# Kernel tuning notes

Hardware: AMD Instinct MI355X
Metric: run time of the kernel (lower is better)

## Reference

```python
import jax, jax.numpy as jnp
import numpy as np

DIM = 1024
E = 8
TOP_K = 2
HID = int(DIM * 2.68)  # 2744


def setup_inputs() -> dict:
    key = jax.random.key(0)
    ks = jax.random.split(key, 8)
    s = 0.02
    return {
        "x": jax.random.normal(ks[0], (4, 1024, DIM), dtype=jnp.float32),
        "gate_w": jax.random.normal(ks[1], (E, DIM), dtype=jnp.float32) * s,
        "w1": jax.random.normal(ks[2], (E, HID, DIM), dtype=jnp.float32) * s,
        "w2": jax.random.normal(ks[3], (E, HID, DIM), dtype=jnp.float32) * s,
        "w3": jax.random.normal(ks[4], (E, DIM, HID), dtype=jnp.float32) * s,
        "sw1": jax.random.normal(ks[5], (HID, DIM), dtype=jnp.float32) * s,
        "sw2": jax.random.normal(ks[6], (HID, DIM), dtype=jnp.float32) * s,
        "sw3": jax.random.normal(ks[7], (DIM, HID), dtype=jnp.float32) * s,
    }


def reference(x, gate_w, w1, w2, w3, sw1, sw2, sw3):
    B, T, C = x.shape
    xf = x.reshape(-1, C)  # [S, C]
    logits = xf @ gate_w.T  # [S, E]
    rw = jax.nn.softmax(logits.astype(jnp.float32), axis=-1)
    tkw, tki = jax.lax.top_k(rw, TOP_K)  # [S, K]
    nE = rw.shape[-1]
    importance = rw.mean(0)  # [E]
    load = jax.nn.one_hot(tki[:, 0], nE, dtype=jnp.float32).mean(0)  # [E]
    aux_loss = nE * (importance * load).sum()
    tkw = tkw / tkw.sum(-1, keepdims=True)
    tkw = tkw.astype(x.dtype)
    # dense all-expert SwiGLU (faithful to original: every expert on every token)
    h = jax.nn.silu(jnp.einsum('sc,ehc->seh', xf, w1)) * jnp.einsum('sc,ehc->seh', xf, w2)  # [S,E,H]
    eo = jnp.einsum('seh,ech->sec', h, w3)  # [S, E, C]
    sel = jnp.take_along_axis(eo, tki[:, :, None], axis=1)  # [S, K, C]
    weighted = (sel * tkw[:, :, None]).sum(1)  # [S, C]
    shared = (jax.nn.silu(xf @ sw1.T) * (xf @ sw2.T)) @ sw3.T  # [S, C]
    y = (weighted + shared).reshape(B, T, C)
    return y, aux_loss
```

## Files before the change

### kernel.cpp

```cpp
#include <hip/hip_runtime.h>
#include <cstdio>
#include <cstdint>

#define S_TOK 4096
#define CDIM  1024
#define EXP   8
#define HRAW  2744
#define HPAD  2816
#define MAXROWS  13312
#define MAXTILES 104
#define NSLICE1  (HPAD / 128)
#define NSLICE2  (CDIM / 256)

typedef __attribute__((ext_vector_type(8))) short bf16x8;
typedef __attribute__((ext_vector_type(4))) float f32x4;
typedef __attribute__((ext_vector_type(4))) unsigned short us4;
typedef unsigned short us;

__device__ __forceinline__ us f2bf(float f) {
  unsigned u = __float_as_uint(f);
  u += 0x7fffu + ((u >> 16) & 1u);
  return (us)(u >> 16);
}

__device__ __forceinline__ void gl16(const us* g, us* l) {
  __builtin_amdgcn_global_load_lds((__attribute__((address_space(1))) void*)g,
                                   (__attribute__((address_space(3))) void*)l,
                                   16, 0, 0);
}

__device__ __forceinline__ int xcd_swz(int orig, int nwg) {
  int q = nwg >> 3, r = nwg & 7;
  int x = orig & 7, idx = orig >> 3;
  return (x < r ? x * (q + 1) : r * (q + 1) + (x - r) * q) + idx;
}

#define CH_RP1  (HPAD * CDIM / 4)
#define CH_CPR  (HPAD / 4)
#define R_W1    (8 * CH_RP1)
#define R_W2    (R_W1 + 8 * CH_RP1)
#define R_W3    (R_W2 + 8 * CDIM * CH_CPR)
#define R_SW1   (R_W3 + CH_RP1)
#define R_SW2   (R_SW1 + CH_RP1)
#define R_SW3   (R_SW2 + CDIM * CH_CPR)
#define GATE_BLKS (S_TOK / 4)
#define CVT_BLKS  2048

__device__ __forceinline__ void cvt4_rowpad(const float* __restrict__ src,
                                            us* __restrict__ dst, int idx) {
  int m = idx / CH_RP1, rem = idx - m * CH_RP1;
  int r = rem >> 8, c4 = rem & 255;
  us4 o;
  if (r < HRAW) {
    float4 v = *(const float4*)(src + ((size_t)(m * HRAW + r) * CDIM + c4 * 4));
    o.x = f2bf(v.x); o.y = f2bf(v.y); o.z = f2bf(v.z); o.w = f2bf(v.w);
  } else { o.x = 0; o.y = 0; o.z = 0; o.w = 0; }
  *(us4*)(dst + ((size_t)(m * HPAD + r) * CDIM + c4 * 4)) = o;
}

__device__ __forceinline__ void cvt4_colpad(const float* __restrict__ src,
                                            us* __restrict__ dst, int idx) {
  int r = idx / CH_CPR, c4 = idx - r * CH_CPR;
  int c = c4 * 4;
  us4 o;
  if (c < HRAW) {
    float4 v = *(const float4*)(src + (size_t)r * HRAW + c);
    o.x = f2bf(v.x); o.y = f2bf(v.y); o.z = f2bf(v.z); o.w = f2bf(v.w);
  } else { o.x = 0; o.y = 0; o.z = 0; o.w = 0; }
  *(us4*)(dst + (size_t)r * HPAD + c) = o;
}

__global__ void __launch_bounds__(256) cvtgate_kernel(
    const float* __restrict__ x, const float* __restrict__ gw,
    const float* __restrict__ w1, const float* __restrict__ w2,
    const float* __restrict__ w3, const float* __restrict__ sw1,
    const float* __restrict__ sw2, const float* __restrict__ sw3,
    us* __restrict__ xb, us* __restrict__ w1b, us* __restrict__ w2b,
    us* __restrict__ w3b, us* __restrict__ sw1b, us* __restrict__ sw2b,
    us* __restrict__ sw3b, int* __restrict__ tki, float* __restrict__ tkw,
    float* __restrict__ probs) {
  if (blockIdx.x < GATE_BLKS) {
    const int wv = threadIdx.x >> 6, lane = threadIdx.x & 63;
    const int s = blockIdx.x * 4 + wv;
    const float4* xs4 = (const float4*)(x + (size_t)s * CDIM);
    float acc[8] = {0, 0, 0, 0, 0, 0, 0, 0};
#pragma unroll
    for (int j = 0; j < 4; j++) {
      float4 v = xs4[lane * 4 + j];
      int c = lane * 16 + j * 4;
      us4 ov;
      ov.x = f2bf(v.x); ov.y = f2bf(v.y); ov.z = f2bf(v.z); ov.w = f2bf(v.w);
      *(us4*)(xb + (size_t)s * CDIM + c) = ov;
#pragma unroll
      for (int ee = 0; ee < 8; ee++) {
        const float* g = gw + ee * CDIM + c;
        acc[ee] += v.x * g[0] + v.y * g[1] + v.z * g[2] + v.w * g[3];
      }
    }
#pragma unroll
    for (int ee = 0; ee < 8; ee++) {
#pragma unroll
      for (int off = 32; off > 0; off >>= 1) acc[ee] += __shfl_xor(acc[ee], off, 64);
    }
    if (lane == 0) {
      float mx = acc[0];
      for (int ee = 1; ee < 8; ee++) mx = fmaxf(mx, acc[ee]);
      float p[8], sm = 0.f;
      for (int ee = 0; ee < 8; ee++) { p[ee] = expf(acc[ee] - mx); sm += p[ee]; }
      float inv = 1.f / sm;
      for (int ee = 0; ee < 8; ee++) probs[s * 8 + ee] = p[ee] * inv;
      int i0 = 0; float b0 = p[0];
      for (int ee = 1; ee < 8; ee++) if (p[ee] > b0) { b0 = p[ee]; i0 = ee; }
      int i1 = -1; float b1 = -1.f;
      for (int ee = 0; ee < 8; ee++) if (ee != i0 && p[ee] > b1) { b1 = p[ee]; i1 = ee; }
      float rw0 = b0 * inv, rw1 = b1 * inv;
      float den = 1.f / (rw0 + rw1);
      tki[2 * s] = i0; tki[2 * s + 1] = i1;
      tkw[2 * s] = rw0 * den; tkw[2 * s + 1] = rw1 * den;
    }
  } else {
    for (int i = (blockIdx.x - GATE_BLKS) * 256 + threadIdx.x; i < R_SW3;
         i += CVT_BLKS * 256) {
      if (i < R_W1)       cvt4_rowpad(w1,  w1b,  i);
      else if (i < R_W2)  cvt4_rowpad(w2,  w2b,  i - R_W1);
      else if (i < R_W3)  cvt4_colpad(w3,  w3b,  i - R_W2);
      else if (i < R_SW1) cvt4_rowpad(sw1, sw1b, i - R_W3);
      else if (i < R_SW2) cvt4_rowpad(sw2, sw2b, i - R_SW1);
      else                cvt4_colpad(sw3, sw3b, i - R_SW2);
    }
  }
}

__global__ void __launch_bounds__(512) build_kernel(const int* __restrict__ tki,
                                                    const float* __restrict__ tkw,
                                                    const float* __restrict__ probs,
                                                    int* __restrict__ meta,
                                                    int* __restrict__ pairtok,
                                                    float* __restrict__ pairw,
                                                    int* __restrict__ invmap,
                                                    int* __restrict__ tile_expert,
                                                    float* __restrict__ aux_out) {
  const int tid = threadIdx.x, lane = tid & 63, wv = tid >> 6;
  __shared__ int s_cnt[EXP];
  __shared__ int s_amc[EXP];
  __shared__ float s_imp[EXP];
  {
    const int e = wv;
    int c_cnt = 0, c_amc = 0;
    float imp = 0.f;
    for (int s0 = 0; s0 < S_TOK; s0 += 64) {
      int s = s0 + lane;
      int i0 = tki[2 * s], i1 = tki[2 * s + 1];
      c_cnt += (i0 == e) || (i1 == e);
      c_amc += (i0 == e);
      imp += probs[s * 8 + e];
    }
#pragma unroll
    for (int off = 32; off > 0; off >>= 1) {
      c_cnt += __shfl_xor(c_cnt, off, 64);
      c_amc += __shfl_xor(c_amc, off, 64);
      imp   += __shfl_xor(imp, off, 64);
    }
    if (lane == 0) { s_cnt[e] = c_cnt; s_amc[e] = c_amc; s_imp[e] = imp; }
  }
  __syncthreads();
  int pad[EXP], start[EXP];
  int o = S_TOK;
#pragma unroll
  for (int j = 0; j < EXP; j++) {
    pad[j] = ((s_cnt[j] + 127) >> 7) << 7;
    start[j] = o;
    o += pad[j];
  }
  const int total = o;
  for (int r = tid; r < S_TOK; r += 512) { pairtok[r] = r; pairw[r] = 1.f; }
  {
    const int e = wv;
    int base = start[e];
    for (int s0 = 0; s0 < S_TOK; s0 += 64) {
      int s = s0 + lane;
      int i0 = tki[2 * s], i1 = tki[2 * s + 1];
      bool m0 = (i0 == e), m1 = (i1 == e);
      bool mm = m0 || m1;
      unsigned long long mk = __ballot(mm);
      if (mm) {
        int pos = base + __popcll(mk & ((1ull << lane) - 1ull));
        pairtok[pos] = s;
        pairw[pos] = m0 ? tkw[2 * s] : tkw[2 * s + 1];
        invmap[2 * s + (m0 ? 0 : 1)] = pos;
      }
      base += __popcll(mk);
    }
    for (int r = base + lane; r < start[e] + pad[e]; r += 64) {
      pairtok[r] = -1; pairw[r] = 0.f;
    }
  }
  if (tid < 128) {
    int ex = 8;
    if (tid >= 32) {
      int rr = tid * 128;
#pragma unroll
      for (int j = 0; j < EXP; j++)
        if (rr >= start[j] && rr < start[j] + pad[j]) ex = j;
    }
    tile_expert[tid] = ex;
  }
  if (tid == 0) {
    meta[0] = total >> 7;
    float a = 0.f;
    for (int j = 0; j < EXP; j++)
      a += (s_imp[j] * (1.f / 4096.f)) * ((float)s_amc[j] * (1.f / 4096.f));
    aux_out[0] = 8.f * a;
  }
}

__global__ void __launch_bounds__(256, 2) gemm1_kernel(
    const us* __restrict__ xb, const us* __restrict__ w1b, const us* __restrict__ w2b,
    const us* __restrict__ sw1b, const us* __restrict__ sw2b,
    const int* __restrict__ pairtok, const int* __restrict__ tile_expert,
    const int* __restrict__ meta, us* __restrict__ h) {
  const int wgid = xcd_swz(blockIdx.x, MAXTILES * NSLICE1);
  const int mt = wgid % MAXTILES;
  if (mt >= meta[0]) return;
  const int n0 = (wgid / MAXTILES) * 128;
  const int e = tile_expert[mt];
  const us* B1 = (e == 8) ? sw1b : (w1b + (size_t)e * HPAD * CDIM);
  const us* B2 = (e == 8) ? sw2b : (w2b + (size_t)e * HPAD * CDIM);
  const int row0 = mt * 128;
  __shared__ __align__(16) us sA[128 * 32];
  __shared__ __align__(16) us sB1[128 * 32];
  __shared__ __align__(16) us sB2[128 * 32];
  const int tid = threadIdx.x, lane = tid & 63;
  const int wm = tid >> 7, wn = (tid >> 6) & 1;
  const int sub = tid & 3, ra = tid >> 2;
  const int subx = sub ^ ((ra >> 1) & 3);
  int t0 = pairtok[row0 + ra];      if (t0 < 0) t0 = 0;
  int t1 = pairtok[row0 + 64 + ra]; if (t1 < 0) t1 = 0;
  const us* gA0 = xb + (size_t)t0 * CDIM + subx * 8;
  const us* gA1 = xb + (size_t)t1 * CDIM + subx * 8;
  const us* gB1a = B1 + (size_t)(n0 + ra) * CDIM + subx * 8;
  const us* gB1b = B1 + (size_t)(n0 + 64 + ra) * CDIM + subx * 8;
  const us* gB2a = B2 + (size_t)(n0 + ra) * CDIM + subx * 8;
  const us* gB2b = B2 + (size_t)(n0 + 64 + ra) * CDIM + subx * 8;
  f32x4 au[4][4], av[4][4];
#pragma unroll
  for (int m = 0; m < 4; m++)
#pragma unroll
    for (int n = 0; n < 4; n++)
#pragma unroll
      for (int r = 0; r < 4; r++) { au[m][n][r] = 0.f; av[m][n][r] = 0.f; }

  const int rl = lane & 15;
  const int kx = (((lane >> 4) ^ ((lane >> 1) & 3)) << 3);
  for (int k0 = 0; k0 < CDIM; k0 += 32) {
    gl16(gA0 + k0,  &sA[tid * 8]);
    gl16(gA1 + k0,  &sA[(tid + 256) * 8]);
    gl16(gB1a + k0, &sB1[tid * 8]);
    gl16(gB1b + k0, &sB1[(tid + 256) * 8]);
    gl16(gB2a + k0, &sB2[tid * 8]);
    gl16(gB2b + k0, &sB2[(tid + 256) * 8]);
    __syncthreads();
    bf16x8 a[4], b1[4], b2[4];
#pragma unroll
    for (int m = 0; m < 4; m++)
      a[m] = *(const bf16x8*)&sA[(wm * 64 + m * 16 + rl) * 32 + kx];
#pragma unroll
    for (int n = 0; n < 4; n++) {
      b1[n] = *(const bf16x8*)&sB1[(wn * 64 + n * 16 + rl) * 32 + kx];
      b2[n] = *(const bf16x8*)&sB2[(wn * 64 + n * 16 + rl) * 32 + kx];
    }
#pragma unroll
    for (int m = 0; m < 4; m++)
#pragma unroll
      for (int n = 0; n < 4; n++) {
        au[m][n] = __builtin_amdgcn_mfma_f32_16x16x32_bf16(a[m], b1[n], au[m][n], 0, 0, 0);
        av[m][n] = __builtin_amdgcn_mfma_f32_16x16x32_bf16(a[m], b2[n], av[m][n], 0, 0, 0);
      }
    __syncthreads();
  }
  const int rb = (lane >> 4) * 4, cb = lane & 15;
#pragma unroll
  for (int m = 0; m < 4; m++)
#pragma unroll
    for (int n = 0; n < 4; n++)
#pragma unroll
      for (int r = 0; r < 4; r++) {
        int row = row0 + wm * 64 + m * 16 + rb + r;
        int col = n0 + wn * 64 + n * 16 + cb;
        float u = au[m][n][r], v = av[m][n][r];
        float sg = 1.f / (1.f + __expf(-u));
        h[(size_t)row * HPAD + col] = f2bf(u * sg * v);
      }
}

__global__ void __launch_bounds__(256, 2) gemm2_kernel(
    const us* __restrict__ h, const us* __restrict__ w3b, const us* __restrict__ sw3b,
    const int* __restrict__ tile_expert, const int* __restrict__ meta,
    float* __restrict__ eo) {
  const int wgid = xcd_swz(blockIdx.x, MAXTILES * NSLICE2);
  const int mt = wgid % MAXTILES;
  if (mt >= meta[0]) return;
  const int n0 = (wgid / MAXTILES) * 256;
  const int e = tile_expert[mt];
  const us* B = (e == 8) ? sw3b : (w3b + (size_t)e * CDIM * HPAD);
  const int row0 = mt * 128;
  __shared__ __align__(16) us sA[128 * 32];
  __shared__ __align__(16) us sB[256 * 32];
  const int tid = threadIdx.x, lane = tid & 63;
  const int wm = tid >> 7, wn = (tid >> 6) & 1;
  const int sub = tid & 3, ra = tid >> 2;
  const int subx = sub ^ ((ra >> 1) & 3);
  const us* gA0 = h + (size_t)(row0 + ra) * HPAD + subx * 8;
  const us* gA1 = h + (size_t)(row0 + 64 + ra) * HPAD + subx * 8;
  const us* gB0 = B + (size_t)(n0 + ra) * HPAD + subx * 8;
  const us* gB1 = B + (size_t)(n0 + 64 + ra) * HPAD + subx * 8;
  const us* gB2 = B + (size_t)(n0 + 128 + ra) * HPAD + subx * 8;
  const us* gB3 = B + (size_t)(n0 + 192 + ra) * HPAD + subx * 8;
  f32x4 ac[4][8];
#pragma unroll
  for (int m = 0; m < 4; m++)
#pragma unroll
    for (int n = 0; n < 8; n++)
#pragma unroll
      for (int r = 0; r < 4; r++) ac[m][n][r] = 0.f;

  const int rl = lane & 15;
  const int kx = (((lane >> 4) ^ ((lane >> 1) & 3)) << 3);
  for (int k0 = 0; k0 < HPAD; k0 += 32) {
    gl16(gA0 + k0, &sA[tid * 8]);
    gl16(gA1 + k0, &sA[(tid + 256) * 8]);
    gl16(gB0 + k0, &sB[tid * 8]);
    gl16(gB1 + k0, &sB[(tid + 256) * 8]);
    gl16(gB2 + k0, &sB[(tid + 512) * 8]);
    gl16(gB3 + k0, &sB[(tid + 768) * 8]);
    __syncthreads();
    bf16x8 a[4], b[8];
#pragma unroll
    for (int m = 0; m < 4; m++)
      a[m] = *(const bf16x8*)&sA[(wm * 64 + m * 16 + rl) * 32 + kx];
#pragma unroll
    for (int n = 0; n < 8; n++)
      b[n] = *(const bf16x8*)&sB[(wn * 128 + n * 16 + rl) * 32 + kx];
#pragma unroll
    for (int m = 0; m < 4; m++)
#pragma unroll
      for (int n = 0; n < 8; n++)
        ac[m][n] = __builtin_amdgcn_mfma_f32_16x16x32_bf16(a[m], b[n], ac[m][n], 0, 0, 0);
    __syncthreads();
  }
  const int rb = (lane >> 4) * 4, cb = lane & 15;
#pragma unroll
  for (int m = 0; m < 4; m++)
#pragma unroll
    for (int n = 0; n < 8; n++)
#pragma unroll
      for (int r = 0; r < 4; r++) {
        int row = row0 + wm * 64 + m * 16 + rb + r;
        int col = n0 + wn * 128 + n * 16 + cb;
        eo[(size_t)row * CDIM + col] = ac[m][n][r];
      }
}

__global__ void __launch_bounds__(256) combine_kernel(const float* __restrict__ eo,
                                                      const int* __restrict__ invmap,
                                                      const float* __restrict__ pairw,
                                                      float* __restrict__ out) {
  const int s = blockIdx.x;
  const int c = threadIdx.x * 4;
  const int j0 = invmap[2 * s], j1 = invmap[2 * s + 1];
  const float w0 = pairw[j0], w1 = pairw[j1];
  float4 a = *(const float4*)(eo + (size_t)s * CDIM + c);
  float4 b = *(const float4*)(eo + (size_t)j0 * CDIM + c);
  float4 d = *(const float4*)(eo + (size_t)j1 * CDIM + c);
  float4 o;
  o.x = a.x + w0 * b.x + w1 * d.x;
  o.y = a.y + w0 * b.y + w1 * d.y;
  o.z = a.z + w0 * b.z + w1 * d.z;
  o.w = a.w + w0 * b.w + w1 * d.w;
  *(float4*)(out + (size_t)s * CDIM + c) = o;
}

extern "C" void kernel_launch(void* const* d_in, const int* in_sizes, int n_in,
                              void* d_out, int out_size, void* d_ws, size_t ws_size,
                              hipStream_t stream) {
  const float* x   = (const float*)d_in[0];
  const float* gw  = (const float*)d_in[1];
  const float* w1  = (const float*)d_in[2];
  const float* w2  = (const float*)d_in[3];
  const float* w3  = (const float*)d_in[4];
  const float* sw1 = (const float*)d_in[5];
  const float* sw2 = (const float*)d_in[6];
  const float* sw3 = (const float*)d_in[7];
  float* out = (float*)d_out;
  char* ws = (char*)d_ws;
  size_t off = 0;
  auto take = [&](size_t bytes) -> char* {
    char* p = ws + off;
    off = (off + bytes + 255) & ~(size_t)255;
    return p;
  };
  us* xb    = (us*)take((size_t)S_TOK * CDIM * 2);
  us* w1b   = (us*)take((size_t)EXP * HPAD * CDIM * 2);
  us* w2b   = (us*)take((size_t)EXP * HPAD * CDIM * 2);
  us* w3b   = (us*)take((size_t)EXP * CDIM * HPAD * 2);
  us* sw1b  = (us*)take((size_t)HPAD * CDIM * 2);
  us* sw2b  = (us*)take((size_t)HPAD * CDIM * 2);
  us* sw3b  = (us*)take((size_t)CDIM * HPAD * 2);
  us* hbuf  = (us*)take((size_t)MAXROWS * HPAD * 2);
  int* pairtok = (int*)take(MAXROWS * 4);
  float* pairw = (float*)take(MAXROWS * 4);
  int* invmap  = (int*)take(S_TOK * 2 * 4);
  int* tile_expert = (int*)take(128 * 4);
  int* tki = (int*)take(S_TOK * 2 * 4);
  float* tkw = (float*)take(S_TOK * 2 * 4);
  float* probs = (float*)take(S_TOK * EXP * 4);
  int* meta = (int*)take(256);
  float* eo = (float*)w1b;
  if (off > ws_size) {
    fprintf(stderr, "MoE kernel: ws too small, need %zu got %zu\n", off, ws_size);
    return;
  }
  cvtgate_kernel<<<GATE_BLKS + CVT_BLKS, 256, 0, stream>>>(
      x, gw, w1, w2, w3, sw1, sw2, sw3,
      xb, w1b, w2b, w3b, sw1b, sw2b, sw3b, tki, tkw, probs);
  build_kernel<<<1, 512, 0, stream>>>(tki, tkw, probs, meta, pairtok, pairw, invmap,
                                      tile_expert, out + (size_t)S_TOK * CDIM);
  gemm1_kernel<<<MAXTILES * NSLICE1, 256, 0, stream>>>(
      xb, w1b, w2b, sw1b, sw2b, pairtok, tile_expert, meta, hbuf);
  gemm2_kernel<<<MAXTILES * NSLICE2, 256, 0, stream>>>(
      hbuf, w3b, sw3b, tile_expert, meta, eo);
  combine_kernel<<<S_TOK, 256, 0, stream>>>(eo, invmap, pairw, out);
}
```

Measured before the change: 472.0 us.

## Overlap weight conversion with routing build and gemm1 via fused launches

```diff
diff --git a/kernel.cpp b/kernel.cpp
--- a/kernel.cpp
+++ b/kernel.cpp
@@ -11,6 +11,7 @@
 #define MAXTILES 104
 #define NSLICE1  (HPAD / 128)
 #define NSLICE2  (CDIM / 256)
+#define G1_BLKS  (MAXTILES * NSLICE1)
 
 typedef __attribute__((ext_vector_type(8))) short bf16x8;
 typedef __attribute__((ext_vector_type(4))) float f32x4;
@@ -37,14 +38,6 @@
 
 #define CH_RP1  (HPAD * CDIM / 4)
 #define CH_CPR  (HPAD / 4)
-#define R_W1    (8 * CH_RP1)
-#define R_W2    (R_W1 + 8 * CH_RP1)
-#define R_W3    (R_W2 + 8 * CDIM * CH_CPR)
-#define R_SW1   (R_W3 + CH_RP1)
-#define R_SW2   (R_SW1 + CH_RP1)
-#define R_SW3   (R_SW2 + CDIM * CH_CPR)
-#define GATE_BLKS (S_TOK / 4)
-#define CVT_BLKS  2048
 
 __device__ __forceinline__ void cvt4_rowpad(const float* __restrict__ src,
                                             us* __restrict__ dst, int idx) {
@@ -70,156 +63,172 @@
   *(us4*)(dst + (size_t)r * HPAD + c) = o;
 }
 
-__global__ void __launch_bounds__(256) cvtgate_kernel(
-    const float* __restrict__ x, const float* __restrict__ gw,
+__global__ void __launch_bounds__(256) gate_kernel(const float* __restrict__ x,
+                                                   const float* __restrict__ gw,
+                                                   us* __restrict__ xb,
+                                                   int* __restrict__ tki,
+                                                   float* __restrict__ tkw,
+                                                   float* __restrict__ probs) {
+  const int wv = threadIdx.x >> 6, lane = threadIdx.x & 63;
+  const int s = blockIdx.x * 4 + wv;
+  const float4* xs4 = (const float4*)(x + (size_t)s * CDIM);
+  float acc[8] = {0, 0, 0, 0, 0, 0, 0, 0};
+#pragma unroll
+  for (int j = 0; j < 4; j++) {
+    float4 v = xs4[lane * 4 + j];
+    int c = lane * 16 + j * 4;
+    us4 ov;
+    ov.x = f2bf(v.x); ov.y = f2bf(v.y); ov.z = f2bf(v.z); ov.w = f2bf(v.w);
+    *(us4*)(xb + (size_t)s * CDIM + c) = ov;
+#pragma unroll
+    for (int ee = 0; ee < 8; ee++) {
+      const float* g = gw + ee * CDIM + c;
+      acc[ee] += v.x * g[0] + v.y * g[1] + v.z * g[2] + v.w * g[3];
+    }
+  }
+#pragma unroll
+  for (int ee = 0; ee < 8; ee++) {
+#pragma unroll
+    for (int off = 32; off > 0; off >>= 1) acc[ee] += __shfl_xor(acc[ee], off, 64);
+  }
+  if (lane == 0) {
+    float mx = acc[0];
+    for (int ee = 1; ee < 8; ee++) mx = fmaxf(mx, acc[ee]);
+    float p[8], sm = 0.f;
+    for (int ee = 0; ee < 8; ee++) { p[ee] = expf(acc[ee] - mx); sm += p[ee]; }
+    float inv = 1.f / sm;
+    for (int ee = 0; ee < 8; ee++) probs[s * 8 + ee] = p[ee] * inv;
+    int i0 = 0; float b0 = p[0];
+    for (int ee = 1; ee < 8; ee++) if (p[ee] > b0) { b0 = p[ee]; i0 = ee; }
+    int i1 = -1; float b1 = -1.f;
+    for (int ee = 0; ee < 8; ee++) if (ee != i0 && p[ee] > b1) { b1 = p[ee]; i1 = ee; }
+    float rw0 = b0 * inv, rw1 = b1 * inv;
+    float den = 1.f / (rw0 + rw1);
+    tki[2 * s] = i0; tki[2 * s + 1] = i1;
+    tkw[2 * s] = rw0 * den; tkw[2 * s + 1] = rw1 * den;
+  }
+}
+
+#define CVTAB_BLKS 2048
+#define AB_W1   (8 * CH_RP1)
+#define AB_W2   (AB_W1 + 8 * CH_RP1)
+#define AB_SW1  (AB_W2 + CH_RP1)
+#define AB_SW2  (AB_SW1 + CH_RP1)
+
+__global__ void __launch_bounds__(512) cvtab_build_kernel(
     const float* __restrict__ w1, const float* __restrict__ w2,
-    const float* __restrict__ w3, const float* __restrict__ sw1,
-    const float* __restrict__ sw2, const float* __restrict__ sw3,
-    us* __restrict__ xb, us* __restrict__ w1b, us* __restrict__ w2b,
-    us* __restrict__ w3b, us* __restrict__ sw1b, us* __restrict__ sw2b,
-    us* __restrict__ sw3b, int* __restrict__ tki, float* __restrict__ tkw,
-    float* __restrict__ probs) {
-  if (blockIdx.x < GATE_BLKS) {
-    const int wv = threadIdx.x >> 6, lane = threadIdx.x & 63;
-    const int s = blockIdx.x * 4 + wv;
-    const float4* xs4 = (const float4*)(x + (size_t)s * CDIM);
-    float acc[8] = {0, 0, 0, 0, 0, 0, 0, 0};
-#pragma unroll
-    for (int j = 0; j < 4; j++) {
-      float4 v = xs4[lane * 4 + j];
-      int c = lane * 16 + j * 4;
-      us4 ov;
-      ov.x = f2bf(v.x); ov.y = f2bf(v.y); ov.z = f2bf(v.z); ov.w = f2bf(v.w);
-      *(us4*)(xb + (size_t)s * CDIM + c) = ov;
-#pragma unroll
-      for (int ee = 0; ee < 8; ee++) {
-        const float* g = gw + ee * CDIM + c;
-        acc[ee] += v.x * g[0] + v.y * g[1] + v.z * g[2] + v.w * g[3];
-      }
-    }
-#pragma unroll
-    for (int ee = 0; ee < 8; ee++) {
-#pragma unroll
-      for (int off = 32; off > 0; off >>= 1) acc[ee] += __shfl_xor(acc[ee], off, 64);
-    }
-    if (lane == 0) {
-      float mx = acc[0];
-      for (int ee = 1; ee < 8; ee++) mx = fmaxf(mx, acc[ee]);
-      float p[8], sm = 0.f;
-      for (int ee = 0; ee < 8; ee++) { p[ee] = expf(acc[ee] - mx); sm += p[ee]; }
-      float inv = 1.f / sm;
-      for (int ee = 0; ee < 8; ee++) probs[s * 8 + ee] = p[ee] * inv;
-      int i0 = 0; float b0 = p[0];
-      for (int ee = 1; ee < 8; ee++) if (p[ee] > b0) { b0 = p[ee]; i0 = ee; }
-      int i1 = -1; float b1 = -1.f;
-      for (int ee = 0; ee < 8; ee++) if (ee != i0 && p[ee] > b1) { b1 = p[ee]; i1 = ee; }
-      float rw0 = b0 * inv, rw1 = b1 * inv;
-      float den = 1.f / (rw0 + rw1);
-      tki[2 * s] = i0; tki[2 * s + 1] = i1;
-      tkw[2 * s] = rw0 * den; tkw[2 * s + 1] = rw1 * den;
-    }
-  } else {
-    for (int i = (blockIdx.x - GATE_BLKS) * 256 + threadIdx.x; i < R_SW3;
-         i += CVT_BLKS * 256) {
-      if (i < R_W1)       cvt4_rowpad(w1,  w1b,  i);
-      else if (i < R_W2)  cvt4_rowpad(w2,  w2b,  i - R_W1);
-      else if (i < R_W3)  cvt4_colpad(w3,  w3b,  i - R_W2);
-      else if (i < R_SW1) cvt4_rowpad(sw1, sw1b, i - R_W3);
-      else if (i < R_SW2) cvt4_rowpad(sw2, sw2b, i - R_SW1);
-      else                cvt4_colpad(sw3, sw3b, i - R_SW2);
-    }
-  }
-}
-
-__global__ void __launch_bounds__(512) build_kernel(const int* __restrict__ tki,
-                                                    const float* __restrict__ tkw,
-                                                    const float* __restrict__ probs,
-                                                    int* __restrict__ meta,
-                                                    int* __restrict__ pairtok,
-                                                    float* __restrict__ pairw,
-                                                    int* __restrict__ invmap,
-                                                    int* __restrict__ tile_expert,
-                                                    float* __restrict__ aux_out) {
-  const int tid = threadIdx.x, lane = tid & 63, wv = tid >> 6;
-  __shared__ int s_cnt[EXP];
-  __shared__ int s_amc[EXP];
-  __shared__ float s_imp[EXP];
-  {
-    const int e = wv;
-    int c_cnt = 0, c_amc = 0;
-    float imp = 0.f;
-    for (int s0 = 0; s0 < S_TOK; s0 += 64) {
-      int s = s0 + lane;
-      int i0 = tki[2 * s], i1 = tki[2 * s + 1];
-      c_cnt += (i0 == e) || (i1 == e);
-      c_amc += (i0 == e);
-      imp += probs[s * 8 + e];
-    }
-#pragma unroll
-    for (int off = 32; off > 0; off >>= 1) {
-      c_cnt += __shfl_xor(c_cnt, off, 64);
-      c_amc += __shfl_xor(c_amc, off, 64);
-      imp   += __shfl_xor(imp, off, 64);
-    }
-    if (lane == 0) { s_cnt[e] = c_cnt; s_amc[e] = c_amc; s_imp[e] = imp; }
-  }
-  __syncthreads();
-  int pad[EXP], start[EXP];
-  int o = S_TOK;
-#pragma unroll
-  for (int j = 0; j < EXP; j++) {
-    pad[j] = ((s_cnt[j] + 127) >> 7) << 7;
-    start[j] = o;
-    o += pad[j];
-  }
-  const int total = o;
-  for (int r = tid; r < S_TOK; r += 512) { pairtok[r] = r; pairw[r] = 1.f; }
-  {
-    const int e = wv;
-    int base = start[e];
-    for (int s0 = 0; s0 < S_TOK; s0 += 64) {
-      int s = s0 + lane;
-      int i0 = tki[2 * s], i1 = tki[2 * s + 1];
-      bool m0 = (i0 == e), m1 = (i1 == e);
-      bool mm = m0 || m1;
-      unsigned long long mk = __ballot(mm);
-      if (mm) {
-        int pos = base + __popcll(mk & ((1ull << lane) - 1ull));
-        pairtok[pos] = s;
-        pairw[pos] = m0 ? tkw[2 * s] : tkw[2 * s + 1];
-        invmap[2 * s + (m0 ? 0 : 1)] = pos;
-      }
-      base += __popcll(mk);
-    }
-    for (int r = base + lane; r < start[e] + pad[e]; r += 64) {
-      pairtok[r] = -1; pairw[r] = 0.f;
-    }
-  }
-  if (tid < 128) {
-    int ex = 8;
-    if (tid >= 32) {
-      int rr = tid * 128;
-#pragma unroll
+    const float* __restrict__ sw1, const float* __restrict__ sw2,
+    us* __restrict__ w1b, us* __restrict__ w2b,
+    us* __restrict__ sw1b, us* __restrict__ sw2b,
+    const int* __restrict__ tki, const float* __restrict__ tkw,
+    const float* __restrict__ probs, int* __restrict__ meta,
+    int* __restrict__ pairtok, float* __restrict__ pairw,
+    int* __restrict__ invmap, int* __restrict__ tile_expert,
+    float* __restrict__ aux_out) {
+  if (blockIdx.x == 0) {
+    const int tid = threadIdx.x, lane = tid & 63, wv = tid >> 6;
+    __shared__ int s_cnt[EXP];
+    __shared__ int s_amc[EXP];
+    __shared__ float s_imp[EXP];
+    {
+      const int e = wv;
+      int c_cnt = 0, c_amc = 0;
+      float imp = 0.f;
+      for (int s0 = 0; s0 < S_TOK; s0 += 64) {
+        int s = s0 + lane;
+        int i0 = tki[2 * s], i1 = tki[2 * s + 1];
+        c_cnt += (i0 == e) || (i1 == e);
+        c_amc += (i0 == e);
+        imp += probs[s * 8 + e];
+      }
+#pragma unroll
+      for (int off = 32; off > 0; off >>= 1) {
+        c_cnt += __shfl_xor(c_cnt, off, 64);
+        c_amc += __shfl_xor(c_amc, off, 64);
+        imp   += __shfl_xor(imp, off, 64);
+      }
+      if (lane == 0) { s_cnt[e] = c_cnt; s_amc[e] = c_amc; s_imp[e] = imp; }
+    }
+    __syncthreads();
+    int pad[EXP], start[EXP];
+    int o = S_TOK;
+#pragma unroll
+    for (int j = 0; j < EXP; j++) {
+      pad[j] = ((s_cnt[j] + 127) >> 7) << 7;
+      start[j] = o;
+      o += pad[j];
+    }
+    const int total = o;
+    for (int r = tid; r < S_TOK; r += 512) { pairtok[r] = r; pairw[r] = 1.f; }
+    {
+      const int e = wv;
+      int base = start[e];
+      for (int s0 = 0; s0 < S_TOK; s0 += 64) {
+        int s = s0 + lane;
+        int i0 = tki[2 * s], i1 = tki[2 * s + 1];
+        bool m0 = (i0 == e), m1 = (i1 == e);
+        bool mm = m0 || m1;
+        unsigned long long mk = __ballot(mm);
+        if (mm) {
+          int pos = base + __popcll(mk & ((1ull << lane) - 1ull));
+          pairtok[pos] = s;
+          pairw[pos] = m0 ? tkw[2 * s] : tkw[2 * s + 1];
+          invmap[2 * s + (m0 ? 0 : 1)] = pos;
+        }
+        base += __popcll(mk);
+      }
+      for (int r = base + lane; r < start[e] + pad[e]; r += 64) {
+        pairtok[r] = -1; pairw[r] = 0.f;
+      }
+    }
+    if (tid < 128) {
+      int ex = 8;
+      if (tid >= 32) {
+        int rr = tid * 128;
+#pragma unroll
+        for (int j = 0; j < EXP; j++)
+          if (rr >= start[j] && rr < start[j] + pad[j]) ex = j;
+      }
+      tile_expert[tid] = ex;
+    }
+    if (tid == 0) {
+      meta[0] = total >> 7;
+      float a = 0.f;
       for (int j = 0; j < EXP; j++)
-        if (rr >= start[j] && rr < start[j] + pad[j]) ex = j;
-    }
-    tile_expert[tid] = ex;
-  }
-  if (tid == 0) {
-    meta[0] = total >> 7;
-    float a = 0.f;
-    for (int j = 0; j < EXP; j++)
-      a += (s_imp[j] * (1.f / 4096.f)) * ((float)s_amc[j] * (1.f / 4096.f));
-    aux_out[0] = 8.f * a;
-  }
-}
+        a += (s_imp[j] * (1.f / 4096.f)) * ((float)s_amc[j] * (1.f / 4096.f));
+      aux_out[0] = 8.f * a;
+    }
+    return;
+  }
+  for (int i = (blockIdx.x - 1) * 512 + threadIdx.x; i < AB_SW2;
+       i += (CVTAB_BLKS - 1) * 512) {
+    if (i < AB_W1)       cvt4_rowpad(w1,  w1b,  i);
+    else if (i < AB_W2)  cvt4_rowpad(w2,  w2b,  i - AB_W1);
+    else if (i < AB_SW1) cvt4_rowpad(sw1, sw1b, i - AB_W2);
+    else                 cvt4_rowpad(sw2, sw2b, i - AB_SW1);
+  }
+}
+
+#define W3CVT_BLKS 1024
+#define W3_CHUNKS  (8 * CDIM * CH_CPR)
+#define W3TOT      (W3_CHUNKS + CDIM * CH_CPR)
 
 __global__ void __launch_bounds__(256, 2) gemm1_kernel(
     const us* __restrict__ xb, const us* __restrict__ w1b, const us* __restrict__ w2b,
     const us* __restrict__ sw1b, const us* __restrict__ sw2b,
     const int* __restrict__ pairtok, const int* __restrict__ tile_expert,
-    const int* __restrict__ meta, us* __restrict__ h) {
-  const int wgid = xcd_swz(blockIdx.x, MAXTILES * NSLICE1);
+    const int* __restrict__ meta, us* __restrict__ h,
+    const float* __restrict__ w3, const float* __restrict__ sw3,
+    us* __restrict__ w3b, us* __restrict__ sw3b) {
+  if (blockIdx.x >= G1_BLKS) {
+    for (int i = (blockIdx.x - G1_BLKS) * 256 + threadIdx.x; i < W3TOT;
+         i += W3CVT_BLKS * 256) {
+      if (i < W3_CHUNKS) cvt4_colpad(w3,  w3b,  i);
+      else               cvt4_colpad(sw3, sw3b, i - W3_CHUNKS);
+    }
+    return;
+  }
+  const int wgid = xcd_swz(blockIdx.x, G1_BLKS);
   const int mt = wgid % MAXTILES;
   if (mt >= meta[0]) return;
   const int n0 = (wgid / MAXTILES) * 128;
@@ -420,13 +429,14 @@
     fprintf(stderr, "MoE kernel: ws too small, need %zu got %zu\n", off, ws_size);
     return;
   }
-  cvtgate_kernel<<<GATE_BLKS + CVT_BLKS, 256, 0, stream>>>(
-      x, gw, w1, w2, w3, sw1, sw2, sw3,
-      xb, w1b, w2b, w3b, sw1b, sw2b, sw3b, tki, tkw, probs);
-  build_kernel<<<1, 512, 0, stream>>>(tki, tkw, probs, meta, pairtok, pairw, invmap,
-                                      tile_expert, out + (size_t)S_TOK * CDIM);
-  gemm1_kernel<<<MAXTILES * NSLICE1, 256, 0, stream>>>(
-      xb, w1b, w2b, sw1b, sw2b, pairtok, tile_expert, meta, hbuf);
+  gate_kernel<<<S_TOK / 4, 256, 0, stream>>>(x, gw, xb, tki, tkw, probs);
+  cvtab_build_kernel<<<CVTAB_BLKS, 512, 0, stream>>>(
+      w1, w2, sw1, sw2, w1b, w2b, sw1b, sw2b,
+      tki, tkw, probs, meta, pairtok, pairw, invmap, tile_expert,
+      out + (size_t)S_TOK * CDIM);
+  gemm1_kernel<<<G1_BLKS + W3CVT_BLKS, 256, 0, stream>>>(
+      xb, w1b, w2b, sw1b, sw2b, pairtok, tile_expert, meta, hbuf,
+      w3, sw3, w3b, sw3b);
   gemm2_kernel<<<MAXTILES * NSLICE2, 256, 0, stream>>>(
       hbuf, w3b, sw3b, tile_expert, meta, eo);
   combine_kernel<<<S_TOK, 256, 0, stream>>>(eo, invmap, pairw, out);
```

New measurement: 429.4 us. -9.0%, faster.
